# Performance work log

Measured on AMD Instinct MI355X. Metric: run time of the kernel, lower is better.

Reference implementation:

```python
import jax, jax.numpy as jnp
import numpy as np
from jax import lax

B, N, C, H, W = 8, 256, 512, 8, 8
DIM = C * 2  # 1024
HW = H * W


def setup_inputs() -> dict:
    key = jax.random.key(0)
    ks = jax.random.split(key, 8)
    x = jax.random.normal(ks[0], (B, N, C, H, W), dtype=jnp.float32)
    # 3 frozen conv1d(1,1,k=5) layers: kaiming-normal weights, zero bias
    conv_w = jax.random.normal(ks[1], (3, 5), dtype=jnp.float32) * np.float32(np.sqrt(2.0 / 5.0))
    conv_b = jnp.zeros((3,), dtype=jnp.float32)
    # 512 tiny Linear(HW, 2): weight [out,in] stacked -> [C, 2, HW], trunc-normal std=0.01
    Ws = (jax.random.truncated_normal(ks[2], -2.0, 2.0, (C, 2, HW), dtype=jnp.float32) * 0.01)
    bs = jnp.zeros((C, 2), dtype=jnp.float32)
    # frozen fc Linear(DIM, DIM)
    fc_w = (jax.random.truncated_normal(ks[3], -2.0, 2.0, (DIM, DIM), dtype=jnp.float32) * 0.01)
    fc_b = jnp.zeros((DIM,), dtype=jnp.float32)
    return {"x": x, "conv_w": conv_w, "conv_b": conv_b, "Ws": Ws, "bs": bs, "fc_w": fc_w, "fc_b": fc_b}


def _conv1d_same(a, w, b):
    # a: [B, N], w: [5], b: scalar; cross-correlation with padding 2 (same as torch Conv1d)
    out = lax.conv_general_dilated(a[:, None, :], w[None, None, :], (1,), [(2, 2)])
    return out[:, 0, :] + b


def reference(x, conv_w, conv_b, Ws, bs, fc_w, fc_b):
    # Channel (patch) attention loop, 3 iterations
    for i in range(3):
        att = x.mean(axis=(2, 3, 4))                      # AdaptiveAvgPool1d(1) over (C H W) -> [B, N]
        att = jax.nn.sigmoid(_conv1d_same(att, conv_w[i], conv_b[i]))  # [B, N]
        x = x * att[:, :, None, None, None]
    xf = x.reshape(B, N, C, HW)
    # 512 per-channel Linear(HW, 2) as one grouped contraction
    y = jnp.einsum('bnch,coh->bnco', xf, Ws) + bs          # [B, N, C, 2]
    y = y.reshape(B, N, C * 2)                             # [B, N, 1024]
    out = y @ fc_w.T + fc_b                                # frozen fc
    # dropout in eval mode = identity
    return out
```

## Files before the change

### kernel.cpp

```cpp
#include <hip/hip_runtime.h>
#include <hip/hip_bf16.h>


typedef unsigned short u16;
typedef unsigned int u32;
typedef __attribute__((ext_vector_type(8))) short short8;
typedef __attribute__((ext_vector_type(4))) float floatx4;

#define Bb 8
#define Nn 256
#define Cc 512
#define HWs 64
#define BN 2048
#define DIMd 1024

__device__ inline u16 f2bf(float f) {
    unsigned int u = __builtin_bit_cast(unsigned int, f);
    unsigned int r = (u + 0x7FFFu + ((u >> 16) & 1u)) >> 16;
    return (u16)r;
}

__global__ __launch_bounds__(256) void k0a_cvt_w(
    const float* __restrict__ w, u16* __restrict__ wb)
{
    const int i = blockIdx.x * 256 + threadIdx.x;
    floatx4 v = ((const floatx4*)w)[i];
    u32 lo = (u32)f2bf(v[0]) | ((u32)f2bf(v[1]) << 16);
    u32 hi = (u32)f2bf(v[2]) | ((u32)f2bf(v[3]) << 16);
    ((u32*)wb)[i * 2 + 0] = lo;
    ((u32*)wb)[i * 2 + 1] = hi;
}

__global__ __launch_bounds__(256) void k0b_bias(
    const float* __restrict__ bs, const float* __restrict__ fc_w,
    const float* __restrict__ fc_b, float* __restrict__ bias2)
{
    const int wv = blockIdx.x * 4 + (threadIdx.x >> 6);
    const int lane = threadIdx.x & 63;
    const floatx4* bp = (const floatx4*)(fc_w + (size_t)wv * DIMd + lane * 16);
    const floatx4* sp = (const floatx4*)(bs + lane * 16);
    float s = 0.f;
    #pragma unroll
    for (int v = 0; v < 4; ++v) {
        floatx4 a = bp[v], b = sp[v];
        #pragma unroll
        for (int j = 0; j < 4; ++j) s += a[j] * b[j];
    }
    #pragma unroll
    for (int sft = 32; sft; sft >>= 1) s += __shfl_xor(s, sft);
    if (lane == 0) bias2[wv] = s + fc_b[wv];
}

__global__ __launch_bounds__(256) void k1_reduce_grouped(
    const float* __restrict__ x, const float* __restrict__ Ws,
    u16* __restrict__ ybf, float* __restrict__ m0)
{
    const int bid = blockIdx.x;
    const int tid = threadIdx.x;
    const float* xb = x + (size_t)bid * (Cc * HWs);
    const int q = tid & 3;
    const int cofs = tid >> 2;
    float lsum = 0.f;

    for (int p = 0; p < 8; ++p) {
        const int c = p * 64 + cofs;
        const floatx4* xp  = (const floatx4*)(xb + p * 4096 + tid * 16);
        const floatx4* w0p = (const floatx4*)(Ws + (size_t)(c * 2 + 0) * HWs + q * 16);
        const floatx4* w1p = (const floatx4*)(Ws + (size_t)(c * 2 + 1) * HWs + q * 16);
        float d0 = 0.f, d1 = 0.f;
        #pragma unroll
        for (int v = 0; v < 4; ++v) {
            floatx4 xv = xp[v];
            floatx4 w0 = w0p[v];
            floatx4 w1 = w1p[v];
            #pragma unroll
            for (int j = 0; j < 4; ++j) {
                d0 += xv[j] * w0[j];
                d1 += xv[j] * w1[j];
                lsum += xv[j];
            }
        }
        d0 += __shfl_xor(d0, 1); d0 += __shfl_xor(d0, 2);
        d1 += __shfl_xor(d1, 1); d1 += __shfl_xor(d1, 2);
        if (q == 0) {
            u32 pk = (u32)f2bf(d0) | ((u32)f2bf(d1) << 16);
            ((u32*)ybf)[(size_t)bid * (DIMd / 2) + c] = pk;
        }
    }
    #pragma unroll
    for (int s = 32; s; s >>= 1) lsum += __shfl_xor(lsum, s);
    __shared__ float wsum[4];
    if ((tid & 63) == 0) wsum[tid >> 6] = lsum;
    __syncthreads();
    if (tid == 0)
        m0[bid] = (wsum[0] + wsum[1] + wsum[2] + wsum[3]) * (1.0f / 32768.f);
}

__global__ __launch_bounds__(256) void k2_scale(
    const float* __restrict__ m0, const float* __restrict__ conv_w,
    const float* __restrict__ conv_b, float* __restrict__ scale)
{
    const int b = blockIdx.x;
    const int n = threadIdx.x;
    __shared__ float buf[Nn];
    float a = m0[b * Nn + n];
    float p = 1.f;
    for (int i = 0; i < 3; ++i) {
        buf[n] = a;
        __syncthreads();
        float t = 0.f;
        #pragma unroll
        for (int k = 0; k < 5; ++k) {
            int idx = n + k - 2;
            float v = (idx >= 0 && idx < Nn) ? buf[idx] : 0.f;
            t += v * conv_w[i * 5 + k];
        }
        t += conv_b[i];
        float s = 1.f / (1.f + __expf(-t));
        p *= s;
        a *= s;
        __syncthreads();
    }
    scale[b * Nn + n] = p;
}

__global__ __launch_bounds__(256) void k3_gemm(
    const u16* __restrict__ ybf, const u16* __restrict__ wbf,
    const float* __restrict__ scale, const float* __restrict__ bias2,
    float* __restrict__ out)
{
    const int tid = threadIdx.x;
    const int w = tid >> 6;
    const int lane = tid & 63;
    const int l15 = lane & 15;
    const int quad = lane >> 4;
    const int wm = w & 1, wn = w >> 1;
    const int r0 = blockIdx.x * 64 + wm * 32;
    const int c0 = blockIdx.y * 64 + wn * 32;

    floatx4 acc[2][2] = {};
    const u16* aptr0 = ybf + (size_t)(r0 + l15) * DIMd + quad * 8;
    const u16* aptr1 = aptr0 + 16 * DIMd;
    const u16* bptr0 = wbf + (size_t)(c0 + l15) * DIMd + quad * 8;
    const u16* bptr1 = bptr0 + 16 * DIMd;

    for (int k0 = 0; k0 < DIMd; k0 += 32) {
        short8 a0 = *(const short8*)(aptr0 + k0);
        short8 a1 = *(const short8*)(aptr1 + k0);
        short8 b0 = *(const short8*)(bptr0 + k0);
        short8 b1 = *(const short8*)(bptr1 + k0);
        acc[0][0] = __builtin_amdgcn_mfma_f32_16x16x32_bf16(a0, b0, acc[0][0], 0, 0, 0);
        acc[0][1] = __builtin_amdgcn_mfma_f32_16x16x32_bf16(a0, b1, acc[0][1], 0, 0, 0);
        acc[1][0] = __builtin_amdgcn_mfma_f32_16x16x32_bf16(a1, b0, acc[1][0], 0, 0, 0);
        acc[1][1] = __builtin_amdgcn_mfma_f32_16x16x32_bf16(a1, b1, acc[1][1], 0, 0, 0);
    }

    #pragma unroll
    for (int ni = 0; ni < 2; ++ni) {
        const int col = c0 + ni * 16 + l15;
        const float b2 = bias2[col];
        #pragma unroll
        for (int mi = 0; mi < 2; ++mi) {
            #pragma unroll
            for (int r = 0; r < 4; ++r) {
                const int row = r0 + mi * 16 + quad * 4 + r;
                out[(size_t)row * DIMd + col] = scale[row] * acc[mi][ni][r] + b2;
            }
        }
    }
}

extern "C" void kernel_launch(void* const* d_in, const int* in_sizes, int n_in,
                              void* d_out, int out_size, void* d_ws, size_t ws_size,
                              hipStream_t stream) {
    const float* x      = (const float*)d_in[0];
    const float* conv_w = (const float*)d_in[1];
    const float* conv_b = (const float*)d_in[2];
    const float* Ws     = (const float*)d_in[3];
    const float* bs     = (const float*)d_in[4];
    const float* fc_w   = (const float*)d_in[5];
    const float* fc_b   = (const float*)d_in[6];
    float* out = (float*)d_out;

    float* m0    = (float*)d_ws;
    float* scale = m0 + BN;
    float* bias2 = scale + BN;
    u16*   ybf   = (u16*)(bias2 + DIMd);
    u16*   wbf   = ybf + (size_t)BN * DIMd;

    k0a_cvt_w<<<dim3(1024), dim3(256), 0, stream>>>(fc_w, wbf);
    k0b_bias<<<dim3(256), dim3(256), 0, stream>>>(bs, fc_w, fc_b, bias2);
    k1_reduce_grouped<<<dim3(BN), dim3(256), 0, stream>>>(x, Ws, ybf, m0);
    k2_scale<<<dim3(Bb), dim3(Nn), 0, stream>>>(m0, conv_w, conv_b, scale);
    k3_gemm<<<dim3(32, 16), dim3(256), 0, stream>>>(ybf, wbf, scale, bias2, out);
}
```

Before: 421.7 us.

## Fuse prep kernels into reduce and GEMM, stage GEMM tiles via async LDS loads

Folds the fc weight bf16 conversion and the bias precompute into the first 256 blocks of the reduction kernel. The conv/sigmoid attention-scale computation moves into the GEMM prologue: each block recomputes its 64-row window using a 6-element halo. The GEMM now double-buffers 64x64 bf16 tiles in XOR-swizzled LDS, filled with global_load_lds. This cuts five launches to two and replaces direct global fragment loads with pipelined shared-memory reuse, at the cost of redundant per-block scale computation and extra syncs.

```diff
diff --git a/kernel.cpp b/kernel.cpp
--- a/kernel.cpp
+++ b/kernel.cpp
@@ -1,11 +1,11 @@
 #include <hip/hip_runtime.h>
-#include <hip/hip_bf16.h>
 
 
 typedef unsigned short u16;
 typedef unsigned int u32;
 typedef __attribute__((ext_vector_type(8))) short short8;
 typedef __attribute__((ext_vector_type(4))) float floatx4;
+typedef __attribute__((ext_vector_type(2))) unsigned int u32x2;
 
 #define Bb 8
 #define Nn 256
@@ -13,47 +13,25 @@
 #define HWs 64
 #define BN 2048
 #define DIMd 1024
-
-__device__ inline u16 f2bf(float f) {
-    unsigned int u = __builtin_bit_cast(unsigned int, f);
-    unsigned int r = (u + 0x7FFFu + ((u >> 16) & 1u)) >> 16;
-    return (u16)r;
-}
-
-__global__ __launch_bounds__(256) void k0a_cvt_w(
-    const float* __restrict__ w, u16* __restrict__ wb)
-{
-    const int i = blockIdx.x * 256 + threadIdx.x;
-    floatx4 v = ((const floatx4*)w)[i];
-    u32 lo = (u32)f2bf(v[0]) | ((u32)f2bf(v[1]) << 16);
-    u32 hi = (u32)f2bf(v[2]) | ((u32)f2bf(v[3]) << 16);
-    ((u32*)wb)[i * 2 + 0] = lo;
-    ((u32*)wb)[i * 2 + 1] = hi;
-}
-
-__global__ __launch_bounds__(256) void k0b_bias(
-    const float* __restrict__ bs, const float* __restrict__ fc_w,
-    const float* __restrict__ fc_b, float* __restrict__ bias2)
-{
-    const int wv = blockIdx.x * 4 + (threadIdx.x >> 6);
-    const int lane = threadIdx.x & 63;
-    const floatx4* bp = (const floatx4*)(fc_w + (size_t)wv * DIMd + lane * 16);
-    const floatx4* sp = (const floatx4*)(bs + lane * 16);
-    float s = 0.f;
-    #pragma unroll
-    for (int v = 0; v < 4; ++v) {
-        floatx4 a = bp[v], b = sp[v];
-        #pragma unroll
-        for (int j = 0; j < 4; ++j) s += a[j] * b[j];
-    }
-    #pragma unroll
-    for (int sft = 32; sft; sft >>= 1) s += __shfl_xor(s, sft);
-    if (lane == 0) bias2[wv] = s + fc_b[wv];
-}
-
-__global__ __launch_bounds__(256) void k1_reduce_grouped(
+#define NT 16
+
+__device__ __forceinline__ u16 f2bf(float f) {
+    u32 u = __builtin_bit_cast(u32, f);
+    return (u16)((u + 0x7FFFu + ((u >> 16) & 1u)) >> 16);
+}
+
+typedef __attribute__((address_space(1))) unsigned int gu32;
+typedef __attribute__((address_space(3))) unsigned int lu32;
+__device__ __forceinline__ void g2l16(const void* g, void* l) {
+    __builtin_amdgcn_global_load_lds((gu32*)g, (lu32*)l, 16, 0, 0);
+}
+
+__global__ __launch_bounds__(256) void k1_fused(
     const float* __restrict__ x, const float* __restrict__ Ws,
-    u16* __restrict__ ybf, float* __restrict__ m0)
+    const float* __restrict__ fc_w, const float* __restrict__ bs,
+    const float* __restrict__ fc_b,
+    u16* __restrict__ ybf, u16* __restrict__ wbf,
+    float* __restrict__ bias2, float* __restrict__ m0)
 {
     const int bid = blockIdx.x;
     const int tid = threadIdx.x;
@@ -94,77 +72,127 @@
     __syncthreads();
     if (tid == 0)
         m0[bid] = (wsum[0] + wsum[1] + wsum[2] + wsum[3]) * (1.0f / 32768.f);
-}
-
-__global__ __launch_bounds__(256) void k2_scale(
+
+    if (bid < 256) {
+        const int wv = bid * 4 + (tid >> 6);
+        const int lane = tid & 63;
+        const floatx4* wp = (const floatx4*)(fc_w + (size_t)wv * DIMd);
+        const floatx4* sp = (const floatx4*)bs;
+        u32x2* wo = (u32x2*)(wbf + (size_t)wv * DIMd);
+        float s = 0.f;
+        #pragma unroll
+        for (int v = 0; v < 4; ++v) {
+            const int j = v * 64 + lane;
+            floatx4 a = wp[j];
+            floatx4 b = sp[j];
+            u32x2 pk;
+            pk[0] = (u32)f2bf(a[0]) | ((u32)f2bf(a[1]) << 16);
+            pk[1] = (u32)f2bf(a[2]) | ((u32)f2bf(a[3]) << 16);
+            wo[j] = pk;
+            s += a[0] * b[0] + a[1] * b[1] + a[2] * b[2] + a[3] * b[3];
+        }
+        #pragma unroll
+        for (int sft = 32; sft; sft >>= 1) s += __shfl_xor(s, sft);
+        if (lane == 0) bias2[wv] = s + fc_b[wv];
+    }
+}
+
+__global__ __launch_bounds__(256) void k3_fused(
+    const u16* __restrict__ ybf, const u16* __restrict__ wbf,
     const float* __restrict__ m0, const float* __restrict__ conv_w,
-    const float* __restrict__ conv_b, float* __restrict__ scale)
-{
-    const int b = blockIdx.x;
-    const int n = threadIdx.x;
-    __shared__ float buf[Nn];
-    float a = m0[b * Nn + n];
-    float p = 1.f;
-    for (int i = 0; i < 3; ++i) {
-        buf[n] = a;
-        __syncthreads();
-        float t = 0.f;
-        #pragma unroll
-        for (int k = 0; k < 5; ++k) {
-            int idx = n + k - 2;
-            float v = (idx >= 0 && idx < Nn) ? buf[idx] : 0.f;
-            t += v * conv_w[i * 5 + k];
-        }
-        t += conv_b[i];
-        float s = 1.f / (1.f + __expf(-t));
-        p *= s;
-        a *= s;
-        __syncthreads();
-    }
-    scale[b * Nn + n] = p;
-}
-
-__global__ __launch_bounds__(256) void k3_gemm(
-    const u16* __restrict__ ybf, const u16* __restrict__ wbf,
-    const float* __restrict__ scale, const float* __restrict__ bias2,
+    const float* __restrict__ conv_b, const float* __restrict__ bias2,
     float* __restrict__ out)
 {
+    __shared__ short8 tiles[2][2][64][8];
+    __shared__ float smA[76], smB[76], sscale[64];
+
     const int tid = threadIdx.x;
-    const int w = tid >> 6;
-    const int lane = tid & 63;
-    const int l15 = lane & 15;
-    const int quad = lane >> 4;
+    const int w = tid >> 6, lane = tid & 63, l15 = lane & 15, quad = lane >> 4;
     const int wm = w & 1, wn = w >> 1;
-    const int r0 = blockIdx.x * 64 + wm * 32;
-    const int c0 = blockIdx.y * 64 + wn * 32;
-
+    const int r0 = blockIdx.x * 64, c0 = blockIdx.y * 64;
+
+    #pragma unroll
+    for (int r = 0; r < 2; ++r) {
+        const int d = r * 256 + tid;
+        const int row = d >> 3, ch = d & 7;
+        const int chs = ch ^ (row & 7);
+        g2l16(ybf + (size_t)(r0 + row) * DIMd + chs * 8, &tiles[0][0][row][ch]);
+        g2l16(wbf + (size_t)(c0 + row) * DIMd + chs * 8, &tiles[0][1][row][ch]);
+    }
+
+    const int bb = r0 >> 8, n0 = r0 & 255;
+    const int gn = n0 - 6 + tid;
+    float a = 0.f, p = 1.f;
+    if (tid < 76) {
+        a = (gn >= 0 && gn < Nn) ? m0[bb * Nn + gn] : 0.f;
+        smA[tid] = a;
+    }
+    __syncthreads();
+    float* cur = smA; float* nxt = smB;
+    for (int i = 0; i < 3; ++i) {
+        if (tid < 76) {
+            float t = conv_b[i];
+            #pragma unroll
+            for (int k = 0; k < 5; ++k) {
+                const int wk = tid + k - 2;
+                const float v = (wk >= 0 && wk < 76) ? cur[wk] : 0.f;
+                t += v * conv_w[i * 5 + k];
+            }
+            const float sg = 1.f / (1.f + __expf(-t));
+            p *= sg;
+            a = (gn >= 0 && gn < Nn) ? a * sg : 0.f;
+            nxt[tid] = a;
+        }
+        __syncthreads();
+        float* tmp = cur; cur = nxt; nxt = tmp;
+    }
+    if (tid >= 6 && tid < 70) sscale[tid - 6] = p;
+
+    const int ar = wm * 32 + l15, br = wn * 32 + l15;
+    const int sA = ar & 7, sB = br & 7;
     floatx4 acc[2][2] = {};
-    const u16* aptr0 = ybf + (size_t)(r0 + l15) * DIMd + quad * 8;
-    const u16* aptr1 = aptr0 + 16 * DIMd;
-    const u16* bptr0 = wbf + (size_t)(c0 + l15) * DIMd + quad * 8;
-    const u16* bptr1 = bptr0 + 16 * DIMd;
-
-    for (int k0 = 0; k0 < DIMd; k0 += 32) {
-        short8 a0 = *(const short8*)(aptr0 + k0);
-        short8 a1 = *(const short8*)(aptr1 + k0);
-        short8 b0 = *(const short8*)(bptr0 + k0);
-        short8 b1 = *(const short8*)(bptr1 + k0);
-        acc[0][0] = __builtin_amdgcn_mfma_f32_16x16x32_bf16(a0, b0, acc[0][0], 0, 0, 0);
-        acc[0][1] = __builtin_amdgcn_mfma_f32_16x16x32_bf16(a0, b1, acc[0][1], 0, 0, 0);
-        acc[1][0] = __builtin_amdgcn_mfma_f32_16x16x32_bf16(a1, b0, acc[1][0], 0, 0, 0);
-        acc[1][1] = __builtin_amdgcn_mfma_f32_16x16x32_bf16(a1, b1, acc[1][1], 0, 0, 0);
+    int cb = 0;
+    for (int kt = 0; kt < NT; ++kt) {
+        if (kt + 1 < NT) {
+            const int nb = cb ^ 1;
+            #pragma unroll
+            for (int r = 0; r < 2; ++r) {
+                const int d = r * 256 + tid;
+                const int row = d >> 3, ch = d & 7;
+                const int chs = ch ^ (row & 7);
+                g2l16(ybf + (size_t)(r0 + row) * DIMd + (kt + 1) * 64 + chs * 8,
+                      &tiles[nb][0][row][ch]);
+                g2l16(wbf + (size_t)(c0 + row) * DIMd + (kt + 1) * 64 + chs * 8,
+                      &tiles[nb][1][row][ch]);
+            }
+        }
+        #pragma unroll
+        for (int ks = 0; ks < 2; ++ks) {
+            const int ca = (quad + ks * 4) ^ sA;
+            const int cbk = (quad + ks * 4) ^ sB;
+            short8 a0 = tiles[cb][0][ar     ][ca];
+            short8 a1 = tiles[cb][0][ar + 16][ca];
+            short8 b0 = tiles[cb][1][br     ][cbk];
+            short8 b1 = tiles[cb][1][br + 16][cbk];
+            acc[0][0] = __builtin_amdgcn_mfma_f32_16x16x32_bf16(a0, b0, acc[0][0], 0, 0, 0);
+            acc[0][1] = __builtin_amdgcn_mfma_f32_16x16x32_bf16(a0, b1, acc[0][1], 0, 0, 0);
+            acc[1][0] = __builtin_amdgcn_mfma_f32_16x16x32_bf16(a1, b0, acc[1][0], 0, 0, 0);
+            acc[1][1] = __builtin_amdgcn_mfma_f32_16x16x32_bf16(a1, b1, acc[1][1], 0, 0, 0);
+        }
+        __syncthreads();
+        cb ^= 1;
     }
 
     #pragma unroll
     for (int ni = 0; ni < 2; ++ni) {
-        const int col = c0 + ni * 16 + l15;
+        const int col = c0 + wn * 32 + ni * 16 + l15;
         const float b2 = bias2[col];
         #pragma unroll
         for (int mi = 0; mi < 2; ++mi) {
             #pragma unroll
             for (int r = 0; r < 4; ++r) {
-                const int row = r0 + mi * 16 + quad * 4 + r;
-                out[(size_t)row * DIMd + col] = scale[row] * acc[mi][ni][r] + b2;
+                const int lr = wm * 32 + mi * 16 + quad * 4 + r;
+                out[(size_t)(r0 + lr) * DIMd + col] = sscale[lr] * acc[mi][ni][r] + b2;
             }
         }
     }
@@ -183,14 +211,10 @@
     float* out = (float*)d_out;
 
     float* m0    = (float*)d_ws;
-    float* scale = m0 + BN;
-    float* bias2 = scale + BN;
+    float* bias2 = m0 + BN;
     u16*   ybf   = (u16*)(bias2 + DIMd);
     u16*   wbf   = ybf + (size_t)BN * DIMd;
 
-    k0a_cvt_w<<<dim3(1024), dim3(256), 0, stream>>>(fc_w, wbf);
-    k0b_bias<<<dim3(256), dim3(256), 0, stream>>>(bs, fc_w, fc_b, bias2);
-    k1_reduce_grouped<<<dim3(BN), dim3(256), 0, stream>>>(x, Ws, ybf, m0);
-    k2_scale<<<dim3(Bb), dim3(Nn), 0, stream>>>(m0, conv_w, conv_b, scale);
-    k3_gemm<<<dim3(32, 16), dim3(256), 0, stream>>>(ybf, wbf, scale, bias2, out);
-}
+    k1_fused<<<dim3(BN), dim3(256), 0, stream>>>(x, Ws, fc_w, bs, fc_b, ybf, wbf, bias2, m0);
+    k3_fused<<<dim3(32, 16), dim3(256), 0, stream>>>(ybf, wbf, m0, conv_w, conv_b, bias2, out);
+}
```

Measured after the change: 396.4 us, median of 2. 1.06x faster.
